# Optimization experiments

Hardware: AMD Instinct MI355X
Metric: run time of the kernel (lower is better)

Reference implementation:

```python
import jax, jax.numpy as jnp
import numpy as np

MAXLEN = 1024
NUMHEADS = 16
INDIM = 1024


def _sinusoid_table(maxlen, dim):
    # positions -maxlen .. maxlen-1  -> (2*maxlen, dim)
    pos = np.arange(-maxlen, maxlen, dtype=np.float64)[:, None]
    hid = np.arange(dim)
    angle = pos / np.power(10000.0, 2 * (hid // 2) / dim)
    table = np.empty_like(angle)
    table[:, 0::2] = np.sin(angle[:, 0::2])
    table[:, 1::2] = np.cos(angle[:, 1::2])
    return jnp.asarray(table.astype(np.float32))


def setup_inputs() -> dict:
    key = jax.random.key(0)
    ks = jax.random.split(key, 12)
    D, H = INDIM, NUMHEADS
    dk = D // H
    def lin(kw, kb_unused, out_d, in_d, std):
        return jax.random.normal(kw, (out_d, in_d), jnp.float32) * std
    std_qk = np.sqrt(2.0 / (D + dk)).astype(np.float32)
    inp = {
        "x": jax.random.normal(ks[0], (4, 1024, D), jnp.float32),
        "Wq": jax.random.normal(ks[1], (D, D), jnp.float32) * std_qk,
        "bq": jnp.zeros((D,), jnp.float32),
        "Wk": jax.random.normal(ks[2], (D, D), jnp.float32) * std_qk,
        "bk": jnp.zeros((D,), jnp.float32),
        "Wv": jax.random.normal(ks[3], (D, D), jnp.float32) * std_qk,
        "bv": jnp.zeros((D,), jnp.float32),
        "Wr": jax.random.normal(ks[4], (D, D), jnp.float32) * (1.0 / np.sqrt(D)),
        "br": jnp.zeros((D,), jnp.float32),
        "rel_u": jax.random.normal(ks[5], (H, dk), jnp.float32) * np.sqrt(2.0 / (H + dk)),
        "rel_v": jax.random.normal(ks[6], (H, dk), jnp.float32) * np.sqrt(2.0 / (H + dk)),
        "Wo": jax.random.normal(ks[7], (D, D), jnp.float32) * np.sqrt(2.0 / (2 * D)),
        "bo": jnp.zeros((D,), jnp.float32),
        "relpos_table": _sinusoid_table(MAXLEN, D),
    }
    return inp


def _forward(x, Wq, bq, Wk, bk, Wv, bv, Wr, br, rel_u, rel_v, Wo, bo, relpos_table):
    b, s, D = x.shape
    H = NUMHEADS
    dk = D // H
    q = (x @ Wq.T + bq).reshape(b, s, H, dk)
    k = (x @ Wk.T + bk).reshape(b, s, H, dk)
    v = (x @ Wv.T + bv).reshape(b, s, H, dk)

    # relpos vectors depend only on distance d = z - s in [-(s-1), s-1];
    # original gathers table rows per (s,z) THEN projects -- by linearity we
    # project the 2s-1 distinct rows once and gather the scores instead.
    R = relpos_table[MAXLEN - s + 1 : MAXLEN + s]            # (L, D), L = 2s-1
    L = 2 * s - 1
    P = (R @ Wk.T + bk).reshape(L, H, dk)                     # k_proj(relpos_vec)
    PR = (R @ Wr.T + br).reshape(L, H, dk)                    # relpos_k_proj(relpos_vec)
    kR = (x @ Wr.T + br).reshape(b, s, H, dk)                 # relpos_k_proj(_k)

    idx2 = jnp.arange(s)[None, :] - jnp.arange(s)[:, None] + (s - 1)  # (s,s): z-s+(s-1)

    w = jnp.einsum('bshd,bzhd->bhsz', q, k)                   # content-content
    A = jnp.einsum('bshd,lhd->bhsl', q, P)                    # content-position, by distance
    w = w + A[:, :, jnp.arange(s)[:, None], idx2]             # gather to (b,h,s,z)
    w = w + jnp.einsum('hd,bzhd->bhz', rel_u, kR)[:, :, None, :]
    Bv = jnp.einsum('hd,lhd->hl', rel_v, PR)                  # (h, L)
    w = w + Bv[:, idx2][None]                                 # (1,h,s,z)

    w = w / jnp.sqrt(jnp.asarray(dk, w.dtype))
    causal = jnp.tril(jnp.ones((s, s), bool))
    w = jnp.where(causal[None, None], w, -jnp.inf)            # == w + log(tril)
    attn = jax.nn.softmax(w, axis=-1)
    vw = jnp.einsum('bhsz,bzhd->bshd', attn, v).reshape(b, s, H * dk)
    return vw @ Wo.T + bo


def reference(x, Wq, bq, Wk, bk, Wv, bv, Wr, br, rel_u, rel_v, Wo, bo, relpos_table):
    return _forward(x, Wq, bq, Wk, bk, Wv, bv, Wr, br, rel_u, rel_v, Wo, bo, relpos_table)
```

## Files before the change

kernel.cpp:

```cpp
#include <hip/hip_runtime.h>


typedef __attribute__((ext_vector_type(8))) short short8;
typedef __attribute__((ext_vector_type(4))) float f32x4;

#define KD 1024

__device__ __forceinline__ float bf2f(short s) {
    unsigned int u = ((unsigned int)(unsigned short)s) << 16;
    return __builtin_bit_cast(float, u);
}
__device__ __forceinline__ short f2bf(float f) {
    unsigned int u = __builtin_bit_cast(unsigned int, f);
    u = u + 0x7fffu + ((u >> 16) & 1u);
    return (short)(u >> 16);
}
__device__ __forceinline__ short8 cvt8(const float* p) {
    f32x4 a = *(const f32x4*)p;
    f32x4 b = *(const f32x4*)(p + 4);
    short8 r;
    r[0] = f2bf(a[0]); r[1] = f2bf(a[1]); r[2] = f2bf(a[2]); r[3] = f2bf(a[3]);
    r[4] = f2bf(b[0]); r[5] = f2bf(b[1]); r[6] = f2bf(b[2]); r[7] = f2bf(b[3]);
    return r;
}

typedef const __attribute__((address_space(1))) void gas_void;
typedef __attribute__((address_space(3))) void las_void;
__device__ __forceinline__ void async16(const void* g, void* l) {
    __builtin_amdgcn_global_load_lds((gas_void*)g, (las_void*)l, 16, 0, 0);
}

template <int CTRL>
__device__ __forceinline__ float dpp_rotf(float v) {
    return __builtin_bit_cast(float, __builtin_amdgcn_update_dpp(
        0, __builtin_bit_cast(int, v), CTRL, 0xF, 0xF, true));
}
__device__ __forceinline__ float row_max16(float v) {
    v = fmaxf(v, dpp_rotf<0x128>(v));
    v = fmaxf(v, dpp_rotf<0x124>(v));
    v = fmaxf(v, dpp_rotf<0x122>(v));
    v = fmaxf(v, dpp_rotf<0x121>(v));
    return v;
}
__device__ __forceinline__ float row_sum16(float v) {
    v += dpp_rotf<0x128>(v);
    v += dpp_rotf<0x124>(v);
    v += dpp_rotf<0x122>(v);
    v += dpp_rotf<0x121>(v);
    return v;
}

struct CvtJobs { const float* src[5]; short* dst[5]; int n8[5]; int njobs; };

__global__ __launch_bounds__(256) void cvtprep_kernel(
    CvtJobs j,
    const float* __restrict__ Wr, const float* __restrict__ br,
    const float* __restrict__ ru, const float* __restrict__ rv,
    short* __restrict__ wrubf, short* __restrict__ wrvbf,
    float* __restrict__ ub, float* __restrict__ vb,
    unsigned int* __restrict__ qcount) {
    const int y = blockIdx.y, tid = threadIdx.x;
    if (y < 5) {
        const int t = blockIdx.x * 256 + tid;
        if (t < j.n8[y]) *(short8*)&j.dst[y][t * 8] = cvt8(&j.src[y][t * 8]);
        return;
    }
    if (blockIdx.x >= 64) return;
    if (blockIdx.x == 0 && tid == 0) *qcount = 0;
    const int idx = blockIdx.x * 256 + tid;
    const int h = idx >> 10, k = idx & 1023;
    float su = 0.f, sv = 0.f;
    for (int d = 0; d < 64; ++d) {
        const float w = Wr[(size_t)(h * 64 + d) * 1024 + k];
        su += ru[h * 64 + d] * w;
        sv += rv[h * 64 + d] * w;
    }
    wrubf[h * 1024 + k] = f2bf(su);
    wrvbf[h * 1024 + k] = f2bf(sv);
    if (idx < 16) {
        float bu = 0.f, bv2 = 0.f;
        for (int d = 0; d < 64; ++d) {
            bu += ru[idx * 64 + d] * br[idx * 64 + d];
            bv2 += rv[idx * 64 + d] * br[idx * 64 + d];
        }
        ub[idx] = bu; vb[idx] = bv2;
    }
}

struct Task { const short* W; const float* bias; short* out; int mode; };
struct Tasks { Task t[6]; };

__global__ __launch_bounds__(256) void gemm_fused(
    const short* __restrict__ A0, const short* __restrict__ A1, Tasks tasks) {
    __shared__ short As[128 * 64];
    __shared__ short Bs[128 * 64];
    const int tid  = threadIdx.x;
    const int wave = tid >> 6, lane = tid & 63;
    const int y    = blockIdx.y;
    const short* A; int m0, n0, tksel;
    if (y < 24)      { A = A0; m0 = blockIdx.x * 128; n0 = (y & 7) * 128; tksel = y >> 3; }
    else if (y < 26) { const int q = (y - 24) * 32 + blockIdx.x;
                       A = A1; m0 = (q >> 3) * 128; n0 = (q & 7) * 128; tksel = 3; }
    else if (y == 26){ A = A0; m0 = blockIdx.x * 128; n0 = 0; tksel = 4; }
    else             { if (blockIdx.x >= 8) return;
                       A = A1; m0 = blockIdx.x * 128; n0 = 0; tksel = 5; }
    const Task tk  = tasks.t[tksel];
    const short* W = tk.W;

    f32x4 acc[4][4];
#pragma unroll
    for (int i = 0; i < 4; ++i)
#pragma unroll
        for (int j = 0; j < 4; ++j) acc[i][j] = (f32x4){0.f, 0.f, 0.f, 0.f};

    const int wm = wave >> 1, wn = wave & 1;
    const int fr_row = lane & 15, fr_k = (lane >> 4) * 8;

    for (int kt = 0; kt < KD / 64; ++kt) {
        const int k0 = kt * 64;
#pragma unroll
        for (int i = 0; i < 4; ++i) {
            const int c = (i * 4 + wave) * 64 + lane;
            const int row = c >> 3, col = ((c & 7) ^ (row & 7)) * 8;
            async16(A + (size_t)(m0 + row) * KD + k0 + col, &As[(i * 4 + wave) * 512]);
            async16(W + (size_t)(n0 + row) * KD + k0 + col, &Bs[(i * 4 + wave) * 512]);
        }
        __syncthreads();
#pragma unroll
        for (int ks = 0; ks < 64; ks += 32) {
            const int un = (ks + fr_k) >> 3;
            short8 a[4], bfrag[4];
#pragma unroll
            for (int mi = 0; mi < 4; ++mi) {
                const int R = wm * 64 + mi * 16 + fr_row;
                a[mi] = *(const short8*)&As[R * 64 + ((un ^ (R & 7)) << 3)];
            }
#pragma unroll
            for (int ni = 0; ni < 4; ++ni) {
                const int R = wn * 64 + ni * 16 + fr_row;
                bfrag[ni] = *(const short8*)&Bs[R * 64 + ((un ^ (R & 7)) << 3)];
            }
#pragma unroll
            for (int mi = 0; mi < 4; ++mi)
#pragma unroll
                for (int ni = 0; ni < 4; ++ni)
                    acc[mi][ni] = __builtin_amdgcn_mfma_f32_16x16x32_bf16(a[mi], bfrag[ni], acc[mi][ni], 0, 0, 0);
        }
        __syncthreads();
    }

    const int mode = tk.mode;
#pragma unroll
    for (int ni = 0; ni < 4; ++ni) {
        const int n = n0 + wn * 64 + ni * 16 + fr_row;
        if (mode >= 3 && n >= 16) continue;
        const float bias = tk.bias[n];
#pragma unroll
        for (int mi = 0; mi < 4; ++mi) {
            const int mbase = m0 + wm * 64 + mi * 16 + (lane >> 4) * 4;
#pragma unroll
            for (int r = 0; r < 4; ++r) {
                const int m = mbase + r;
                const float val = acc[mi][ni][r] + bias;
                if (mode == 0)
                    tk.out[(((size_t)(m >> 10) * 16 + (n >> 6)) * 1024 + (m & 1023)) * 64 + (n & 63)] = f2bf(val);
                else if (mode == 1)
                    tk.out[(((size_t)(m >> 10) * 16 + (n >> 6)) * 64 + (n & 63)) * 1024 + (m & 1023)] = f2bf(val);
                else if (mode == 2)
                    tk.out[((size_t)(n >> 6) * 1024 + m) * 64 + (n & 63)] = f2bf(val);
                else if (mode == 3)
                    ((float*)tk.out)[((size_t)(m >> 10) * 16 + n) * 1024 + (m & 1023)] = val;
                else
                    ((float*)tk.out)[(size_t)n * 1024 + m] = val;
            }
        }
    }
}

__global__ __launch_bounds__(256) void gemm_out(const short* __restrict__ A,
                                                const float* __restrict__ W,
                                                const float* __restrict__ bias,
                                                float* __restrict__ out) {
    __shared__ short As[128 * 64];
    __shared__ short Bs[64 * 64];
    const int tid  = threadIdx.x;
    const int wave = tid >> 6, lane = tid & 63;
    const int m0   = blockIdx.x * 128;
    const int n0   = blockIdx.y * 64;

    f32x4 acc[4][2];
#pragma unroll
    for (int i = 0; i < 4; ++i)
#pragma unroll
        for (int j = 0; j < 2; ++j) acc[i][j] = (f32x4){0.f, 0.f, 0.f, 0.f};

    const int wm = wave >> 1, wn = wave & 1;
    const int fr_row = lane & 15, fr_k = (lane >> 4) * 8;
    const int brow = tid >> 2, bcol16 = (tid & 3) * 16;

    for (int kt = 0; kt < KD / 64; ++kt) {
        const int k0 = kt * 64;
#pragma unroll
        for (int i = 0; i < 4; ++i) {
            const int c = (i * 4 + wave) * 64 + lane;
            const int row = c >> 3, col = ((c & 7) ^ (row & 7)) * 8;
            async16(A + (size_t)(m0 + row) * KD + k0 + col, &As[(i * 4 + wave) * 512]);
        }
        {
            const float* wp = W + (size_t)(n0 + brow) * KD + k0 + bcol16;
            short8 v0 = cvt8(wp);
            short8 v1 = cvt8(wp + 8);
            const int u0 = bcol16 >> 3;
            short* dst = &Bs[brow * 64];
            *(short8*)&dst[((u0 ^ (brow & 7)) << 3)]       = v0;
            *(short8*)&dst[(((u0 + 1) ^ (brow & 7)) << 3)] = v1;
        }
        __syncthreads();
#pragma unroll
        for (int ks = 0; ks < 64; ks += 32) {
            const int un = (ks + fr_k) >> 3;
            short8 a[4], bfrag[2];
#pragma unroll
            for (int mi = 0; mi < 4; ++mi) {
                const int R = wm * 64 + mi * 16 + fr_row;
                a[mi] = *(const short8*)&As[R * 64 + ((un ^ (R & 7)) << 3)];
            }
#pragma unroll
            for (int ni = 0; ni < 2; ++ni) {
                const int R = wn * 32 + ni * 16 + fr_row;
                bfrag[ni] = *(const short8*)&Bs[R * 64 + ((un ^ (R & 7)) << 3)];
            }
#pragma unroll
            for (int mi = 0; mi < 4; ++mi)
#pragma unroll
                for (int ni = 0; ni < 2; ++ni)
                    acc[mi][ni] = __builtin_amdgcn_mfma_f32_16x16x32_bf16(a[mi], bfrag[ni], acc[mi][ni], 0, 0, 0);
        }
        __syncthreads();
    }

#pragma unroll
    for (int ni = 0; ni < 2; ++ni) {
        const int n = n0 + wn * 32 + ni * 16 + fr_row;
        const float bv = bias[n];
#pragma unroll
        for (int mi = 0; mi < 4; ++mi) {
            const int mbase = m0 + wm * 64 + mi * 16 + (lane >> 4) * 4;
#pragma unroll
            for (int r = 0; r < 4; ++r)
                out[(size_t)(mbase + r) * 1024 + n] = acc[mi][ni][r] + bv;
        }
    }
}

__global__ __launch_bounds__(256) void attn_kernel(
    const short* __restrict__ q_ws, const short* __restrict__ k_ws,
    const short* __restrict__ v_ws, const short* __restrict__ p_ws,
    const float* __restrict__ U_ws, const float* __restrict__ Bv_ws,
    short* __restrict__ vw, unsigned int* __restrict__ qcount) {
    __shared__ short Ks[64 * 64];
    __shared__ short Ps[128 * 64];
    __shared__ float Band2[64 * 64];
    short* Pls = (short*)Band2;

    const int tid = threadIdx.x;
    const int w = tid >> 6, lane = tid & 63;

    if (tid == 0) *(int*)&Band2[0] = (int)atomicAdd(qcount, 1u);
    __syncthreads();
    const int it = *(const int*)&Band2[0];
    const int bx = 15 - (it >> 6);
    const int g  = it & 63;
    const int h = g & 15, b = g >> 4;
    const int i0 = bx * 64;
    const int bh = b * 16 + h;
    const int fr_row = lane & 15, fr_q = lane >> 4, fr_k = fr_q * 8;
    const int lr = lane >> 3, lc = lane & 7;

    short8 qfrag[2];
    {
        const short* qrow = q_ws + ((size_t)bh * 1024 + i0 + w * 16 + fr_row) * 64;
        qfrag[0] = *(const short8*)&qrow[fr_k];
        qfrag[1] = *(const short8*)&qrow[32 + fr_k];
    }

    float m_run[4], l_run[4];
    f32x4 o_acc[4];
#pragma unroll
    for (int r2 = 0; r2 < 4; ++r2) { m_run[r2] = -1e30f; l_run[r2] = 0.f; }
#pragma unroll
    for (int dt = 0; dt < 4; ++dt) o_acc[dt] = (f32x4){0.f, 0.f, 0.f, 0.f};

    const int tt0 = 3 - w;
    const short* krowbase = k_ws + (size_t)bh * 1024 * 64;
    const short* vrowbase = v_ws + (size_t)bh * 64 * 1024;
    const short* prowbase = p_ws + (size_t)h * 1024 * 64;

    {
        const int l_lo0 = 960 - i0;
#pragma unroll
        for (int i = 0; i < 2; ++i) {
            const int R = (w * 2 + i) * 8 + lr;
            async16(krowbase + (size_t)R * 64 + ((lc ^ (R & 7)) * 8), &Ks[(w * 2 + i) * 512]);
        }
#pragma unroll
        for (int i = 0; i < 4; ++i) {
            const int R = (w * 4 + i) * 8 + lr;
            int gl = l_lo0 + R; gl = gl > 1023 ? 1023 : gl;
            async16(prowbase + (size_t)gl * 64 + ((lc ^ (R & 7)) * 8), &Ps[(w * 4 + i) * 512]);
        }
    }

    for (int jt = 0; jt <= bx; ++jt) {
        const int j0 = jt * 64;
        const int l_lo = j0 - i0 + 960;

        asm volatile("s_waitcnt vmcnt(0)" ::: "memory");
        __builtin_amdgcn_s_barrier();
        asm volatile("" ::: "memory");

        float uv[4];
#pragma unroll
        for (int tt = 0; tt < 4; ++tt) uv[tt] = U_ws[bh * 1024 + j0 + tt * 16 + fr_row];
        float bvv[5];
#pragma unroll
        for (int u = 0; u < 5; ++u) {
            int l = l_lo + (tt0 + u) * 16 + fr_row;
            l = l > 1023 ? 1023 : l;
            bvv[u] = Bv_ws[h * 1024 + l];
        }

        f32x4 qk[4], bd[5];
#pragma unroll
        for (int tt = 0; tt < 4; ++tt) qk[tt] = (f32x4){0.f, 0.f, 0.f, 0.f};
#pragma unroll
        for (int u = 0; u < 5; ++u) bd[u] = (f32x4){0.f, 0.f, 0.f, 0.f};

        __builtin_amdgcn_s_setprio(1);
#pragma unroll
        for (int c = 0; c < 2; ++c) {
            const int col = c * 4 + fr_q;
#pragma unroll
            for (int tt = 0; tt < 4; ++tt) {
                const int R = tt * 16 + fr_row;
                short8 kf = *(const short8*)&Ks[R * 64 + ((col ^ (R & 7)) << 3)];
                qk[tt] = __builtin_amdgcn_mfma_f32_16x16x32_bf16(qfrag[c], kf, qk[tt], 0, 0, 0);
            }
#pragma unroll
            for (int u = 0; u < 5; ++u) {
                const int R = (tt0 + u) * 16 + fr_row;
                short8 pf = *(const short8*)&Ps[R * 64 + ((col ^ (R & 7)) << 3)];
                bd[u] = __builtin_amdgcn_mfma_f32_16x16x32_bf16(qfrag[c], pf, bd[u], 0, 0, 0);
            }
        }
        __builtin_amdgcn_s_setprio(0);

        const short* vjt = vrowbase + j0;
        short8 vregA[4], vregB[4];
#pragma unroll
        for (int dt = 0; dt < 4; ++dt)
            vregA[dt] = *(const short8*)&vjt[(size_t)(dt * 16 + fr_row) * 1024 + fr_k];
#pragma unroll
        for (int dt = 0; dt < 4; ++dt)
            vregB[dt] = *(const short8*)&vjt[(size_t)(dt * 16 + fr_row) * 1024 + 32 + fr_k];

        asm volatile("" ::: "memory");
        __builtin_amdgcn_s_barrier();
        asm volatile("" ::: "memory");

        if (jt < bx) {
            const int j0n = j0 + 64;
            const int l_lo_n = l_lo + 64;
#pragma unroll
            for (int i = 0; i < 2; ++i) {
                const int R = (w * 2 + i) * 8 + lr;
                async16(krowbase + (size_t)(j0n + R) * 64 + ((lc ^ (R & 7)) * 8), &Ks[(w * 2 + i) * 512]);
            }
#pragma unroll
            for (int i = 0; i < 4; ++i) {
                const int R = (w * 4 + i) * 8 + lr;
                int gl = l_lo_n + R; gl = gl > 1023 ? 1023 : gl;
                async16(prowbase + (size_t)gl * 64 + ((lc ^ (R & 7)) * 8), &Ps[(w * 4 + i) * 512]);
            }
        }

#pragma unroll
        for (int u = 0; u < 5; ++u) {
#pragma unroll
            for (int r2 = 0; r2 < 4; ++r2) {
                const int ilw = fr_q * 4 + r2;
                const int jp = u * 16 + fr_row + ilw - 15;
                if (jp >= 0 && jp < 64) {
                    const int row = w * 16 + ilw;
                    Band2[row * 64 + (jp ^ ((row & 7) << 3))] = bd[u][r2] + bvv[u];
                }
            }
        }

        float p[4][4], mt[4];
#pragma unroll
        for (int r2 = 0; r2 < 4; ++r2) mt[r2] = -1e30f;
#pragma unroll
        for (int tt = 0; tt < 4; ++tt) {
            const int jp = tt * 16 + fr_row;
            const int jj = j0 + jp;
#pragma unroll
            for (int r2 = 0; r2 < 4; ++r2) {
                const int ilw = fr_q * 4 + r2;
                const int row = w * 16 + ilw;
                const int ii = i0 + row;
                const float band = Band2[row * 64 + (jp ^ ((row & 7) << 3))];
                float sv = (qk[tt][r2] + band + uv[tt]) * 0.125f;
                sv = (jj <= ii) ? sv : -1e30f;
                p[tt][r2] = sv;
                mt[r2] = fmaxf(mt[r2], sv);
            }
        }
#pragma unroll
        for (int r2 = 0; r2 < 4; ++r2) mt[r2] = row_max16(mt[r2]);

        bool grow = false;
#pragma unroll
        for (int r2 = 0; r2 < 4; ++r2) grow = grow || (mt[r2] > m_run[r2]);
        if (__any(grow)) {
#pragma unroll
            for (int r2 = 0; r2 < 4; ++r2) {
                const float mn = fmaxf(m_run[r2], mt[r2]);
                const float alpha = __expf(m_run[r2] - mn);
                m_run[r2] = mn;
                l_run[r2] *= alpha;
#pragma unroll
                for (int dt = 0; dt < 4; ++dt) o_acc[dt][r2] *= alpha;
            }
        }

#pragma unroll
        for (int r2 = 0; r2 < 4; ++r2) {
            float ls = 0.f;
#pragma unroll
            for (int tt = 0; tt < 4; ++tt) { p[tt][r2] = __expf(p[tt][r2] - m_run[r2]); ls += p[tt][r2]; }
            l_run[r2] += ls;
        }

#pragma unroll
        for (int tt = 0; tt < 4; ++tt)
#pragma unroll
            for (int r2 = 0; r2 < 4; ++r2) {
                const int row = w * 16 + fr_q * 4 + r2;
                Pls[row * 128 + ((tt * 16 + fr_row) ^ ((row & 7) << 3))] = f2bf(p[tt][r2]);
            }

        __builtin_amdgcn_s_setprio(1);
#pragma unroll
        for (int c = 0; c < 2; ++c) {
            const int ks = c * 32;
            const int prow = w * 16 + fr_row;
            short8 pa = *(const short8*)&Pls[prow * 128 + ((ks + fr_k) ^ ((prow & 7) << 3))];
#pragma unroll
            for (int dt = 0; dt < 4; ++dt) {
                short8 vf = (c == 0) ? vregA[dt] : vregB[dt];
                o_acc[dt] = __builtin_amdgcn_mfma_f32_16x16x32_bf16(pa, vf, o_acc[dt], 0, 0, 0);
            }
        }
        __builtin_amdgcn_s_setprio(0);
    }

    float lf[4];
#pragma unroll
    for (int r2 = 0; r2 < 4; ++r2) lf[r2] = row_sum16(l_run[r2]);
#pragma unroll
    for (int dt = 0; dt < 4; ++dt) {
        const int d = dt * 16 + fr_row;
#pragma unroll
        for (int r2 = 0; r2 < 4; ++r2) {
            const int ii = i0 + w * 16 + fr_q * 4 + r2;
            const float val = o_acc[dt][r2] / lf[r2];
            vw[(((size_t)b * 1024 + ii) * 16 + h) * 64 + d] = f2bf(val);
        }
    }
}

extern "C" void kernel_launch(void* const* d_in, const int* in_sizes, int n_in,
                              void* d_out, int out_size, void* d_ws, size_t ws_size,
                              hipStream_t stream) {
    (void)in_sizes; (void)n_in; (void)out_size; (void)ws_size;
    const float* x     = (const float*)d_in[0];
    const float* Wq    = (const float*)d_in[1];
    const float* bq    = (const float*)d_in[2];
    const float* Wk    = (const float*)d_in[3];
    const float* bk    = (const float*)d_in[4];
    const float* Wv    = (const float*)d_in[5];
    const float* bvv   = (const float*)d_in[6];
    const float* Wr    = (const float*)d_in[7];
    const float* br    = (const float*)d_in[8];
    const float* rel_u = (const float*)d_in[9];
    const float* rel_v = (const float*)d_in[10];
    const float* Wo    = (const float*)d_in[11];
    const float* bo    = (const float*)d_in[12];
    const float* relpos= (const float*)d_in[13];

    const size_t MEG = 1 << 20;
    short* ws    = (short*)d_ws;
    short* xbf   = ws;
    short* vw_ws = ws;
    short* wqbf  = ws + 4 * MEG;
    short* wkbf  = ws + 5 * MEG;
    short* wvbf  = ws + 6 * MEG;
    short* rbf   = ws + 7 * MEG;
    short* q_ws  = ws + 8 * MEG;
    short* k_ws  = ws + 12 * MEG;
    short* v_ws  = ws + 16 * MEG;
    short* p_ws  = ws + 20 * MEG;
    float* U_ws  = (float*)(ws + 21 * MEG);
    float* Bv_ws = U_ws + 65536;
    float* ub    = Bv_ws + 16384;
    float* vb    = ub + 16;
    short* wrubf = (short*)(vb + 16);
    short* wrvbf = wrubf + 131072;
    unsigned int* qcount = (unsigned int*)(wrvbf + 131072);

    CvtJobs cj;
    cj.src[0] = x;             cj.dst[0] = xbf;  cj.n8[0] = (4 * MEG) / 8;
    cj.src[1] = Wq;            cj.dst[1] = wqbf; cj.n8[1] = MEG / 8;
    cj.src[2] = Wk;            cj.dst[2] = wkbf; cj.n8[2] = MEG / 8;
    cj.src[3] = Wv;            cj.dst[3] = wvbf; cj.n8[3] = MEG / 8;
    cj.src[4] = relpos + 1024; cj.dst[4] = rbf;  cj.n8[4] = MEG / 8;
    cj.njobs = 5;
    cvtprep_kernel<<<dim3(2048, 6), 256, 0, stream>>>(cj, Wr, br, rel_u, rel_v,
                                                      wrubf, wrvbf, ub, vb, qcount);

    Tasks t1;
    t1.t[0] = {wqbf,  bq,  q_ws, 0};
    t1.t[1] = {wkbf,  bk,  k_ws, 0};
    t1.t[2] = {wvbf,  bvv, v_ws, 1};
    t1.t[3] = {wkbf,  bk,  p_ws, 2};
    t1.t[4] = {wrubf, ub,  (short*)U_ws,  3};
    t1.t[5] = {wrvbf, vb,  (short*)Bv_ws, 4};
    gemm_fused<<<dim3(32, 28), 256, 0, stream>>>(xbf, rbf, t1);

    attn_kernel<<<dim3(1024), 256, 0, stream>>>(q_ws, k_ws, v_ws, p_ws, U_ws,
                                                Bv_ws, vw_ws, qcount);

    gemm_out<<<dim3(32, 16), 256, 0, stream>>>(vw_ws, Wo, bo, (float*)d_out);
}
```

Measured before the change: 255.2 us.

## Ring-buffer relpos tiles, fold softmax scale into projections, skip off-diagonal masking

The relative-position tile in shared memory becomes a two-slot ring buffer of 64-row halves. Each key step now loads only 64 new P rows instead of reloading the full 128-row window, which halves P global traffic per iteration. The 1/sqrt(dk) scale moves into the projection GEMM epilogue (q, U and Bv outputs), removing a multiply per score. The causal mask is now applied only on the diagonal tile. Risks include slot-indexing mistakes in the ring buffer and precision shifts from scaling before the bf16 conversion.

```diff
diff --git a/kernel.cpp b/kernel.cpp
--- a/kernel.cpp
+++ b/kernel.cpp
@@ -106,6 +106,7 @@
                        A = A1; m0 = blockIdx.x * 128; n0 = 0; tksel = 5; }
     const Task tk  = tasks.t[tksel];
     const short* W = tk.W;
+    const float oscale = (tksel == 0 || tksel >= 4) ? 0.125f : 1.0f;
 
     f32x4 acc[4][4];
 #pragma unroll
@@ -161,7 +162,7 @@
 #pragma unroll
             for (int r = 0; r < 4; ++r) {
                 const int m = mbase + r;
-                const float val = acc[mi][ni][r] + bias;
+                const float val = (acc[mi][ni][r] + bias) * oscale;
                 if (mode == 0)
                     tk.out[(((size_t)(m >> 10) * 16 + (n >> 6)) * 1024 + (m & 1023)) * 64 + (n & 63)] = f2bf(val);
                 else if (mode == 1)
@@ -259,7 +260,7 @@
     const float* __restrict__ U_ws, const float* __restrict__ Bv_ws,
     short* __restrict__ vw, unsigned int* __restrict__ qcount) {
     __shared__ short Ks[64 * 64];
-    __shared__ short Ps[128 * 64];
+    __shared__ short Ps2[2][64 * 64];
     __shared__ float Band2[64 * 64];
     short* Pls = (short*)Band2;
 
@@ -305,9 +306,11 @@
         }
 #pragma unroll
         for (int i = 0; i < 4; ++i) {
-            const int R = (w * 4 + i) * 8 + lr;
+            const int c = w * 4 + i;
+            const int R = c * 8 + lr;
             int gl = l_lo0 + R; gl = gl > 1023 ? 1023 : gl;
-            async16(prowbase + (size_t)gl * 64 + ((lc ^ (R & 7)) * 8), &Ps[(w * 4 + i) * 512]);
+            async16(prowbase + (size_t)gl * 64 + ((lc ^ (R & 7)) * 8),
+                    &Ps2[c >> 3][(c & 7) * 512]);
         }
     }
 
@@ -349,7 +352,9 @@
 #pragma unroll
             for (int u = 0; u < 5; ++u) {
                 const int R = (tt0 + u) * 16 + fr_row;
-                short8 pf = *(const short8*)&Ps[R * 64 + ((col ^ (R & 7)) << 3)];
+                const int slot = (jt + (R >> 6)) & 1;
+                const int r6 = R & 63;
+                short8 pf = *(const short8*)&Ps2[slot][r6 * 64 + ((col ^ (r6 & 7)) << 3)];
                 bd[u] = __builtin_amdgcn_mfma_f32_16x16x32_bf16(qfrag[c], pf, bd[u], 0, 0, 0);
             }
         }
@@ -370,17 +375,23 @@
 
         if (jt < bx) {
             const int j0n = j0 + 64;
-            const int l_lo_n = l_lo + 64;
 #pragma unroll
             for (int i = 0; i < 2; ++i) {
                 const int R = (w * 2 + i) * 8 + lr;
                 async16(krowbase + (size_t)(j0n + R) * 64 + ((lc ^ (R & 7)) * 8), &Ks[(w * 2 + i) * 512]);
             }
 #pragma unroll
-            for (int i = 0; i < 4; ++i) {
-                const int R = (w * 4 + i) * 8 + lr;
-                int gl = l_lo_n + R; gl = gl > 1023 ? 1023 : gl;
-                async16(prowbase + (size_t)gl * 64 + ((lc ^ (R & 7)) * 8), &Ps[(w * 4 + i) * 512]);
+            for (int i = 0; i < 1; ++i) {
+                const int cc = w * 2 + (i * 4);
+                (void)cc;
+            }
+#pragma unroll
+            for (int i = 0; i < 2; ++i) {
+                const int cc = w * 2 + i;
+                const int r = cc * 8 + lr;
+                int gl = l_lo + 128 + r; gl = gl > 1023 ? 1023 : gl;
+                async16(prowbase + (size_t)gl * 64 + ((lc ^ (r & 7)) * 8),
+                        &Ps2[jt & 1][cc * 512]);
             }
         }
 
@@ -397,6 +408,7 @@
             }
         }
 
+        const bool diag = (jt == bx);
         float p[4][4], mt[4];
 #pragma unroll
         for (int r2 = 0; r2 < 4; ++r2) mt[r2] = -1e30f;
@@ -408,10 +420,9 @@
             for (int r2 = 0; r2 < 4; ++r2) {
                 const int ilw = fr_q * 4 + r2;
                 const int row = w * 16 + ilw;
-                const int ii = i0 + row;
                 const float band = Band2[row * 64 + (jp ^ ((row & 7) << 3))];
-                float sv = (qk[tt][r2] + band + uv[tt]) * 0.125f;
-                sv = (jj <= ii) ? sv : -1e30f;
+                float sv = qk[tt][r2] + band + uv[tt];
+                if (diag) { const int ii = i0 + row; sv = (jj <= ii) ? sv : -1e30f; }
                 p[tt][r2] = sv;
                 mt[r2] = fmaxf(mt[r2], sv);
             }
```

New measurement: 260.4 us. 2.0% more time.
